# Optimization experiments

Measured on AMD Instinct MI355X. Metric: run time of the kernel, lower is better.

## Reference

```python
import jax, jax.numpy as jnp
import numpy as np

B, S, D = 2, 2048, 1024
H, DH = 16, 64  # num_head, head_dim; H*DH == D


def setup_inputs() -> dict:
    key = jax.random.key(0)
    ks = jax.random.split(key, 10)
    stdv = 1.0 / np.sqrt(D)
    def lin(k):
        kw, kb = jax.random.split(k)
        W = jax.random.uniform(kw, (D, D), jnp.float32, -stdv, stdv)
        b = jax.random.uniform(kb, (D,), jnp.float32, -stdv, stdv)
        return W, b
    Wq, bq = lin(ks[0]); Wk, bk = lin(ks[1]); Wv, bv = lin(ks[2]); Wo, bo = lin(ks[3])
    x = jax.random.normal(ks[4], (B, S, D), jnp.float32)
    # causal mask: True = attend
    mask = jnp.tril(jnp.ones((S, S), jnp.bool_))
    mask = jnp.broadcast_to(mask, (B, S, S))
    return {"x": x, "mask": mask, "Wq": Wq, "bq": bq, "Wk": Wk, "bk": bk,
            "Wv": Wv, "bv": bv, "Wo": Wo, "bo": bo}


def _split_head(t):
    # [B,S,D] -> [B*H, S, DH]
    return t.reshape(B, S, H, DH).transpose(0, 2, 1, 3).reshape(B * H, S, DH)


def _concat_head(t):
    # [B*H, S, DH] -> [B, S, D]
    return t.reshape(B, H, S, DH).transpose(0, 2, 1, 3).reshape(B, S, D)


def reference(x, mask, Wq, bq, Wk, bk, Wv, bv, Wo, bo):
    q = _split_head(x @ Wq.T + bq)
    k = _split_head(x @ Wk.T + bk)
    v = _split_head(x @ Wv.T + bv)
    scale = 1.0 / jnp.sqrt(jnp.float32(DH))
    # scores: [B, H, S, S], masked softmax (flash-attention math, unfused ref)
    scores = jnp.einsum('nqd,nkd->nqk', q, k).reshape(B, H, S, S) * scale
    scores = jnp.where(mask[:, None, :, :], scores, jnp.finfo(scores.dtype).min)
    attn = jax.nn.softmax(scores, axis=-1)
    out = jnp.einsum('bhqk,nkd->bhqd', attn, v.reshape(B, H, S, DH).reshape(B * H, S, DH)).reshape(B * H, S, DH) if False else jnp.einsum('nqk,nkd->nqd', attn.reshape(B * H, S, S), v)
    return _concat_head(out) @ Wo.T + bo
```

## Files before the change

### kernel.cpp

```cpp
#include <hip/hip_runtime.h>
#include <cstdint>

#define S_LEN  2048
#define NH     16
#define DHEAD  64
#define DMODEL 1024

typedef __bf16 bf16x8 __attribute__((ext_vector_type(8)));
typedef __bf16 bf16x2 __attribute__((ext_vector_type(2)));
typedef float  f32x4  __attribute__((ext_vector_type(4)));

__device__ __forceinline__ unsigned short f2bf(float x) {
  union { float f; unsigned int u; } c; c.f = x;
  unsigned int u = c.u;
  return (unsigned short)((u + 0x7fffu + ((u >> 16) & 1u)) >> 16);
}

__device__ __forceinline__ unsigned int pkbf(float a, float b) {
#if __has_builtin(__builtin_amdgcn_cvt_pk_bf16_f32)
  bf16x2 r = __builtin_amdgcn_cvt_pk_bf16_f32(a, b);
  return *(unsigned int*)&r;
#else
  return (unsigned int)f2bf(a) | ((unsigned int)f2bf(b) << 16);
#endif
}

__device__ __forceinline__ unsigned short f2bf1(float x) {
#if __has_builtin(__builtin_amdgcn_cvt_pk_bf16_f32)
  bf16x2 r = __builtin_amdgcn_cvt_pk_bf16_f32(x, x);
  union { bf16x2 v; unsigned int u; } c; c.v = r;
  return (unsigned short)(c.u & 0xffffu);
#else
  return f2bf(x);
#endif
}

__device__ __forceinline__ __bf16 us2bf(unsigned short u) {
  union { unsigned short u; __bf16 b; } c; c.u = u; return c.b;
}

__device__ __forceinline__ void glds16(const void* g, void* l) {
  __builtin_amdgcn_global_load_lds(
      (const __attribute__((address_space(1))) void*)g,
      (__attribute__((address_space(3))) void*)l, 16, 0, 0);
}

__device__ __forceinline__ f32x4 mfma16(bf16x8 a, bf16x8 b, f32x4 c) {
  return __builtin_amdgcn_mfma_f32_16x16x32_bf16(a, b, c, 0, 0, 0);
}

__global__ void cvt_all(const float* __restrict__ x,
                        const float* __restrict__ Wq,
                        const float* __restrict__ Wk,
                        const float* __restrict__ Wv,
                        const float* __restrict__ Wo,
                        unsigned short* __restrict__ xb,
                        unsigned short* __restrict__ wqkv,
                        unsigned short* __restrict__ wo) {
  const int b = blockIdx.x;
  const float* src;
  unsigned short* dst;
  int off;
  if (b < 4096)      { src = x;  dst = xb;                off = b; }
  else if (b < 5120) { src = Wq; dst = wqkv;              off = b - 4096; }
  else if (b < 6144) { src = Wk; dst = wqkv + (1 << 20);  off = b - 5120; }
  else if (b < 7168) { src = Wv; dst = wqkv + (2 << 20);  off = b - 6144; }
  else               { src = Wo; dst = wo;                off = b - 7168; }
  const int i = (off * 256 + threadIdx.x) * 4;
  float4 v = *(const float4*)&src[i];
  uint2 r;
  r.x = pkbf(v.x, v.y);
  r.y = pkbf(v.z, v.w);
  *(uint2*)&dst[i] = r;
}

template<int MODE, int BN>
__global__ __launch_bounds__(256)
void gemm_bt(const unsigned short* __restrict__ A,
             const unsigned short* __restrict__ W,
             const float* __restrict__ bias0,
             const float* __restrict__ bias1,
             const float* __restrict__ bias2,
             unsigned short* __restrict__ Qt,
             unsigned short* __restrict__ Kb,
             unsigned short* __restrict__ Vt,
             float* __restrict__ Out,
             int K) {
  constexpr int JN = BN / 32;
  __shared__ __align__(16) unsigned short As[2][128 * 32];
  __shared__ __align__(16) unsigned short Bs[2][BN * 32];
  const int t    = threadIdx.x;
  const int lane = t & 63;
  const int w    = t >> 6;
  const int lr   = lane & 15, lq = lane >> 4;
  const int wm   = (w >> 1) * 64, wn = (w & 1) * (BN / 2);
  const int m0   = blockIdx.y * 128, n0 = blockIdx.x * BN;
  const int ra   = t >> 2, ca = (t & 3) * 8;

  f32x4 acc[4][JN] = {};

  const int niter = K >> 6;
  for (int kk = 0; kk < niter; ++kk) {
    const int k0 = kk << 6;
#pragma unroll
    for (int kh = 0; kh < 2; ++kh) {
      const int kc = k0 + kh * 32;
      glds16(A + (m0 + ra) * K + kc + ca,      &As[kh][ra * 32 + ca]);
      glds16(A + (m0 + 64 + ra) * K + kc + ca, &As[kh][(64 + ra) * 32 + ca]);
      glds16(W + (n0 + ra) * K + kc + ca,      &Bs[kh][ra * 32 + ca]);
      if (BN == 128)
        glds16(W + (n0 + 64 + ra) * K + kc + ca, &Bs[kh][(64 + ra) * 32 + ca]);
    }
    __syncthreads();
#pragma unroll
    for (int kh = 0; kh < 2; ++kh) {
      bf16x8 af[4], bg[JN];
#pragma unroll
      for (int i = 0; i < 4; ++i)
        af[i] = *(const bf16x8*)&As[kh][(wm + i * 16 + lr) * 32 + lq * 8];
#pragma unroll
      for (int j = 0; j < JN; ++j)
        bg[j] = *(const bf16x8*)&Bs[kh][(wn + j * 16 + lr) * 32 + lq * 8];
#pragma unroll
      for (int i = 0; i < 4; ++i)
#pragma unroll
        for (int j = 0; j < JN; ++j)
          acc[i][j] = mfma16(af[i], bg[j], acc[i][j]);
    }
    __syncthreads();
  }

  if (MODE == 0) {
    const int tsel = n0 >> 10;
#pragma unroll
    for (int i = 0; i < 4; ++i) {
#pragma unroll
      for (int j = 0; j < JN; ++j) {
        const int mb = m0 + wm + i * 16 + lq * 4;
        const int n  = n0 + wn + j * 16 + lr;
        const int d  = n & 1023;
        const int bidx = mb >> 11, s = mb & (S_LEN - 1);
        const int h = d >> 6, dh = d & 63;
        const int bh = bidx * NH + h;
        const float bv0 = (tsel == 0) ? bias0[d] : ((tsel == 1) ? bias1[d] : bias2[d]);
        if (tsel == 0) {
          const float sc = 0.125f * 1.44269504088896f;
          uint2 pv;
          pv.x = pkbf((acc[i][j][0] + bv0) * sc, (acc[i][j][1] + bv0) * sc);
          pv.y = pkbf((acc[i][j][2] + bv0) * sc, (acc[i][j][3] + bv0) * sc);
          *(uint2*)&Qt[(bh * DHEAD + dh) * S_LEN + s] = pv;
        } else if (tsel == 2) {
          uint2 pv;
          pv.x = pkbf(acc[i][j][0] + bv0, acc[i][j][1] + bv0);
          pv.y = pkbf(acc[i][j][2] + bv0, acc[i][j][3] + bv0);
          *(uint2*)&Vt[(bh * DHEAD + dh) * S_LEN + s] = pv;
        } else {
#pragma unroll
          for (int r = 0; r < 4; ++r)
            Kb[(bh * S_LEN + s + r) * DHEAD + dh] = f2bf1(acc[i][j][r] + bv0);
        }
      }
    }
  } else {
#pragma unroll
    for (int i = 0; i < 4; ++i)
#pragma unroll
      for (int j = 0; j < JN; ++j)
#pragma unroll
        for (int r = 0; r < 4; ++r) {
          const int m = m0 + wm + i * 16 + lq * 4 + r;
          const int n = n0 + wn + j * 16 + lr;
          Out[m * DMODEL + n] = acc[i][j][r] + bias0[n];
        }
  }
}

__global__ __launch_bounds__(256, 2)
void flash_kernel(const unsigned short* __restrict__ Qt,
                  const unsigned short* __restrict__ Kb,
                  const unsigned short* __restrict__ Vt,
                  unsigned short* __restrict__ Ocat) {
  __shared__ __align__(16) unsigned short Ks[2][2][2][64 * 32];
  __shared__ __align__(16) unsigned short Vs[2][2][2][64 * 32];
  __shared__ __align__(16) unsigned short pls[4][1024];
  const int w = threadIdx.x >> 6, lane = threadIdx.x & 63;
  const int lr = lane & 15, lq = lane >> 4;
  const int bh = blockIdx.x;
  const int pp = blockIdx.y;
  const char* Kc = (const char*)(Kb + bh * (S_LEN * DHEAD));
  const char* Vc = (const char*)(Vt + bh * (DHEAD * S_LEN));
  const unsigned short* Qp = Qt + bh * (DHEAD * S_LEN);
  const int bb = bh >> 4, h = bh & 15;
  unsigned short* pw = &pls[w][0];
  const int swz = lr & 7;

  const int hh  = w & 1;
  const int rbb = (w >> 1) * 2;
  const int rlane = lane >> 2;
  const int slane = lane & 3;
  const int swslot = (slane ^ ((rlane >> 1) & 3)) * 16;
  const int rsw = (lq ^ ((lr >> 1) & 3)) * 8;

  bf16x8 ones;
#pragma unroll
  for (int j = 0; j < 8; ++j) ones[j] = (__bf16)1.0f;

  auto run_strip = [&](int sb) {
    const int nbt = (sb + 2) >> 1;
    const int q0 = sb * 64 + w * 16;
    bf16x8 qlo, qhi;
#pragma unroll
    for (int j = 0; j < 8; ++j) {
      qlo[j] = us2bf(Qp[(lq * 8 + j) * S_LEN + q0 + lr]);
      qhi[j] = us2bf(Qp[(32 + lq * 8 + j) * S_LEN + q0 + lr]);
    }
    f32x4 o[4] = {};
    f32x4 lacc = {};

    auto stage = [&](int buf, int bt) {
#pragma unroll
      for (int sub = 0; sub < 2; ++sub) {
        const int sk0 = bt * 128 + sub * 64;
#pragma unroll
        for (int j = 0; j < 2; ++j) {
          const int rb = rbb + j;
          glds16(Kc + (sk0 + rb * 16 + rlane) * 128 + hh * 64 + swslot,
                 &Ks[buf][sub][hh][rb * 16 * 32]);
          glds16(Vc + (rb * 16 + rlane) * 4096 + (sk0 + hh * 32) * 2 + swslot,
                 &Vs[buf][sub][hh][rb * 16 * 32]);
        }
      }
    };

    stage(0, 0);
    for (int bt = 0; bt < nbt; ++bt) {
      const int buf = bt & 1;
      __syncthreads();
      if (bt + 1 < nbt) stage(1 - buf, bt + 1);

#pragma unroll
      for (int sub = 0; sub < 2; ++sub) {
        f32x4 st[4] = {};
        const unsigned short* Kl = Ks[buf][sub][0];
        const unsigned short* Kh = Ks[buf][sub][1];
#pragma unroll
        for (int t = 0; t < 4; ++t) {
          st[t] = mfma16(*(const bf16x8*)&Kl[(t * 16 + lr) * 32 + rsw], qlo, st[t]);
          st[t] = mfma16(*(const bf16x8*)&Kh[(t * 16 + lr) * 32 + rsw], qhi, st[t]);
        }
        float p[4][4];
#pragma unroll
        for (int t = 0; t < 4; ++t)
#pragma unroll
          for (int r = 0; r < 4; ++r)
            p[t][r] = __builtin_amdgcn_exp2f(st[t][r]);
        if (bt == nbt - 1) {
          const int q = q0 + lr, sk0 = bt * 128 + sub * 64;
#pragma unroll
          for (int t = 0; t < 4; ++t)
#pragma unroll
            for (int r = 0; r < 4; ++r) {
              const int k = sk0 + t * 16 + lq * 4 + r;
              if (k > q) p[t][r] = 0.f;
            }
        }

#pragma unroll
        for (int t = 0; t < 4; ++t) {
          uint2 pk;
          pk.x = pkbf(p[t][0], p[t][1]);
          pk.y = pkbf(p[t][2], p[t][3]);
          const int g = t * 2 + (lq >> 1);
          *(uint2*)&pw[lr * 64 + ((g ^ swz) << 3) + ((lq & 1) << 2)] = pk;
        }
        const bf16x8 pf0 = *(const bf16x8*)&pw[lr * 64 + ((lq ^ swz) << 3)];
        const bf16x8 pf1 = *(const bf16x8*)&pw[lr * 64 + (((4 + lq) ^ swz) << 3)];
        const unsigned short* Vl = Vs[buf][sub][0];
        const unsigned short* Vh = Vs[buf][sub][1];
#pragma unroll
        for (int tt = 0; tt < 4; ++tt) {
          o[tt] = mfma16(*(const bf16x8*)&Vl[(tt * 16 + lr) * 32 + rsw], pf0, o[tt]);
          o[tt] = mfma16(*(const bf16x8*)&Vh[(tt * 16 + lr) * 32 + rsw], pf1, o[tt]);
        }
        lacc = mfma16(ones, pf0, lacc);
        lacc = mfma16(ones, pf1, lacc);
      }
    }

    const float inv = 1.f / lacc[0];
#pragma unroll
    for (int tt = 0; tt < 4; ++tt) {
      uint2 ov;
      ov.x = pkbf(o[tt][0] * inv, o[tt][1] * inv);
      ov.y = pkbf(o[tt][2] * inv, o[tt][3] * inv);
      *(uint2*)&Ocat[(bb * S_LEN + q0 + lr) * DMODEL + h * DHEAD + tt * 16 + lq * 4] = ov;
    }
    __syncthreads();
  };

  run_strip(31 - pp);
  run_strip(pp);
}

extern "C" void kernel_launch(void* const* d_in, const int* in_sizes, int n_in,
                              void* d_out, int out_size, void* d_ws, size_t ws_size,
                              hipStream_t stream) {
  const float* x  = (const float*)d_in[0];
  const float* Wq = (const float*)d_in[2];
  const float* bq = (const float*)d_in[3];
  const float* Wk = (const float*)d_in[4];
  const float* bk = (const float*)d_in[5];
  const float* Wv = (const float*)d_in[6];
  const float* bv = (const float*)d_in[7];
  const float* Wo = (const float*)d_in[8];
  const float* bo = (const float*)d_in[9];
  float* out = (float*)d_out;

  char* ws = (char*)d_ws;
  unsigned short* xb   = (unsigned short*)(ws);
  unsigned short* wqkv = (unsigned short*)(ws + (8ull  << 20));
  unsigned short* wo   = (unsigned short*)(ws + (14ull << 20));
  unsigned short* Qt   = (unsigned short*)(ws + (16ull << 20));
  unsigned short* Kb   = (unsigned short*)(ws + (24ull << 20));
  unsigned short* Vt   = (unsigned short*)(ws + (32ull << 20));
  unsigned short* Ocat = (unsigned short*)(ws + (40ull << 20));

  cvt_all<<<8192, 256, 0, stream>>>(x, Wq, Wk, Wv, Wo, xb, wqkv, wo);

  gemm_bt<0, 128><<<dim3(24, 32), 256, 0, stream>>>(xb, wqkv, bq, bk, bv,
                                                    Qt, Kb, Vt, nullptr, 1024);
  flash_kernel<<<dim3(32, 16), 256, 0, stream>>>(Qt, Kb, Vt, Ocat);
  gemm_bt<1, 64><<<dim3(16, 32), 256, 0, stream>>>(Ocat, wo, bo, nullptr, nullptr,
                                                   nullptr, nullptr, nullptr, out, 1024);
}
```

Before: 204.4 us.

## Split flash attention key tiles across warps and reduce partial outputs in LDS

```diff
diff --git a/kernel.cpp b/kernel.cpp
--- a/kernel.cpp
+++ b/kernel.cpp
@@ -180,9 +180,8 @@
                   const unsigned short* __restrict__ Kb,
                   const unsigned short* __restrict__ Vt,
                   unsigned short* __restrict__ Ocat) {
-  __shared__ __align__(16) unsigned short Ks[2][2][2][64 * 32];
-  __shared__ __align__(16) unsigned short Vs[2][2][2][64 * 32];
-  __shared__ __align__(16) unsigned short pls[4][1024];
+  __shared__ __align__(16) float Msh[4][64 * 64];
+  __shared__ float Ml[4][64];
   const int w = threadIdx.x >> 6, lane = threadIdx.x & 63;
   const int lr = lane & 15, lq = lane >> 4;
   const int bh = blockIdx.x;
@@ -191,62 +190,51 @@
   const char* Vc = (const char*)(Vt + bh * (DHEAD * S_LEN));
   const unsigned short* Qp = Qt + bh * (DHEAD * S_LEN);
   const int bb = bh >> 4, h = bh & 15;
-  unsigned short* pw = &pls[w][0];
+  unsigned short* pw = (unsigned short*)&Msh[w][0];
   const int swz = lr & 7;
 
-  const int hh  = w & 1;
-  const int rbb = (w >> 1) * 2;
-  const int rlane = lane >> 2;
-  const int slane = lane & 3;
-  const int swslot = (slane ^ ((rlane >> 1) & 3)) * 16;
-  const int rsw = (lq ^ ((lr >> 1) & 3)) * 8;
-
   bf16x8 ones;
 #pragma unroll
   for (int j = 0; j < 8; ++j) ones[j] = (__bf16)1.0f;
 
   auto run_strip = [&](int sb) {
-    const int nbt = (sb + 2) >> 1;
-    const int q0 = sb * 64 + w * 16;
-    bf16x8 qlo, qhi;
-#pragma unroll
-    for (int j = 0; j < 8; ++j) {
-      qlo[j] = us2bf(Qp[(lq * 8 + j) * S_LEN + q0 + lr]);
-      qhi[j] = us2bf(Qp[(32 + lq * 8 + j) * S_LEN + q0 + lr]);
-    }
-    f32x4 o[4] = {};
-    f32x4 lacc = {};
-
-    auto stage = [&](int buf, int bt) {
-#pragma unroll
-      for (int sub = 0; sub < 2; ++sub) {
-        const int sk0 = bt * 128 + sub * 64;
-#pragma unroll
-        for (int j = 0; j < 2; ++j) {
-          const int rb = rbb + j;
-          glds16(Kc + (sk0 + rb * 16 + rlane) * 128 + hh * 64 + swslot,
-                 &Ks[buf][sub][hh][rb * 16 * 32]);
-          glds16(Vc + (rb * 16 + rlane) * 4096 + (sk0 + hh * 32) * 2 + swslot,
-                 &Vs[buf][sub][hh][rb * 16 * 32]);
-        }
-      }
-    };
-
-    stage(0, 0);
-    for (int bt = 0; bt < nbt; ++bt) {
-      const int buf = bt & 1;
-      __syncthreads();
-      if (bt + 1 < nbt) stage(1 - buf, bt + 1);
-
-#pragma unroll
-      for (int sub = 0; sub < 2; ++sub) {
+    const int len = sb + 1;
+    const int q0 = sb * 64;
+    bf16x8 qlo[4], qhi[4];
+#pragma unroll
+    for (int qg = 0; qg < 4; ++qg)
+#pragma unroll
+      for (int j = 0; j < 8; ++j) {
+        qlo[qg][j] = us2bf(Qp[(lq * 8 + j) * S_LEN + q0 + qg * 16 + lr]);
+        qhi[qg][j] = us2bf(Qp[(32 + lq * 8 + j) * S_LEN + q0 + qg * 16 + lr]);
+      }
+    f32x4 o[4][4] = {};
+    f32x4 lacc[4] = {};
+
+    for (int kt = w; kt < len; kt += 4) {
+      const int sk0 = kt << 6;
+      bf16x8 kf0[4], kf1[4];
+#pragma unroll
+      for (int t = 0; t < 4; ++t) {
+        const char* kr = Kc + (sk0 + t * 16 + lr) * 128 + lq * 16;
+        kf0[t] = *(const bf16x8*)(kr);
+        kf1[t] = *(const bf16x8*)(kr + 64);
+      }
+      bf16x8 vf0[4], vf1[4];
+#pragma unroll
+      for (int tt = 0; tt < 4; ++tt) {
+        const char* vr = Vc + (tt * 16 + lr) * 4096 + sk0 * 2 + lq * 16;
+        vf0[tt] = *(const bf16x8*)(vr);
+        vf1[tt] = *(const bf16x8*)(vr + 64);
+      }
+      const bool diag = (kt == len - 1);
+#pragma unroll
+      for (int qg = 0; qg < 4; ++qg) {
         f32x4 st[4] = {};
-        const unsigned short* Kl = Ks[buf][sub][0];
-        const unsigned short* Kh = Ks[buf][sub][1];
 #pragma unroll
         for (int t = 0; t < 4; ++t) {
-          st[t] = mfma16(*(const bf16x8*)&Kl[(t * 16 + lr) * 32 + rsw], qlo, st[t]);
-          st[t] = mfma16(*(const bf16x8*)&Kh[(t * 16 + lr) * 32 + rsw], qhi, st[t]);
+          st[t] = mfma16(kf0[t], qlo[qg], st[t]);
+          st[t] = mfma16(kf1[t], qhi[qg], st[t]);
         }
         float p[4][4];
 #pragma unroll
@@ -254,8 +242,8 @@
 #pragma unroll
           for (int r = 0; r < 4; ++r)
             p[t][r] = __builtin_amdgcn_exp2f(st[t][r]);
-        if (bt == nbt - 1) {
-          const int q = q0 + lr, sk0 = bt * 128 + sub * 64;
+        if (diag) {
+          const int q = q0 + qg * 16 + lr;
 #pragma unroll
           for (int t = 0; t < 4; ++t)
 #pragma unroll
@@ -264,36 +252,53 @@
               if (k > q) p[t][r] = 0.f;
             }
         }
-
+        const int prow = (qg * 16 + lr) * 64;
 #pragma unroll
         for (int t = 0; t < 4; ++t) {
           uint2 pk;
           pk.x = pkbf(p[t][0], p[t][1]);
           pk.y = pkbf(p[t][2], p[t][3]);
           const int g = t * 2 + (lq >> 1);
-          *(uint2*)&pw[lr * 64 + ((g ^ swz) << 3) + ((lq & 1) << 2)] = pk;
-        }
-        const bf16x8 pf0 = *(const bf16x8*)&pw[lr * 64 + ((lq ^ swz) << 3)];
-        const bf16x8 pf1 = *(const bf16x8*)&pw[lr * 64 + (((4 + lq) ^ swz) << 3)];
-        const unsigned short* Vl = Vs[buf][sub][0];
-        const unsigned short* Vh = Vs[buf][sub][1];
+          *(uint2*)&pw[prow + ((g ^ swz) << 3) + ((lq & 1) << 2)] = pk;
+        }
+        const bf16x8 pf0 = *(const bf16x8*)&pw[prow + ((lq ^ swz) << 3)];
+        const bf16x8 pf1 = *(const bf16x8*)&pw[prow + (((4 + lq) ^ swz) << 3)];
 #pragma unroll
         for (int tt = 0; tt < 4; ++tt) {
-          o[tt] = mfma16(*(const bf16x8*)&Vl[(tt * 16 + lr) * 32 + rsw], pf0, o[tt]);
-          o[tt] = mfma16(*(const bf16x8*)&Vh[(tt * 16 + lr) * 32 + rsw], pf1, o[tt]);
-        }
-        lacc = mfma16(ones, pf0, lacc);
-        lacc = mfma16(ones, pf1, lacc);
-      }
-    }
-
-    const float inv = 1.f / lacc[0];
-#pragma unroll
-    for (int tt = 0; tt < 4; ++tt) {
+          o[qg][tt] = mfma16(vf0[tt], pf0, o[qg][tt]);
+          o[qg][tt] = mfma16(vf1[tt], pf1, o[qg][tt]);
+        }
+        lacc[qg] = mfma16(ones, pf0, lacc[qg]);
+        lacc[qg] = mfma16(ones, pf1, lacc[qg]);
+      }
+    }
+
+#pragma unroll
+    for (int qg = 0; qg < 4; ++qg) {
+#pragma unroll
+      for (int tt = 0; tt < 4; ++tt) {
+        const int slot = (tt * 4 + lq) ^ lr;
+        *(f32x4*)&Msh[w][(qg * 16 + lr) * 64 + slot * 4] = o[qg][tt];
+      }
+      if (lq == 0) Ml[w][qg * 16 + lr] = lacc[qg][0];
+    }
+    __syncthreads();
+    const int qrow = w * 16 + lr;
+    const float lt = Ml[0][qrow] + Ml[1][qrow] + Ml[2][qrow] + Ml[3][qrow];
+    const float inv = 1.f / lt;
+#pragma unroll
+    for (int m = 0; m < 4; ++m) {
+      const int slot = (m * 4 + lq) ^ lr;
+      f32x4 s = *(const f32x4*)&Msh[0][qrow * 64 + slot * 4];
+#pragma unroll
+      for (int v = 1; v < 4; ++v) {
+        f32x4 r = *(const f32x4*)&Msh[v][qrow * 64 + slot * 4];
+        s = s + r;
+      }
       uint2 ov;
-      ov.x = pkbf(o[tt][0] * inv, o[tt][1] * inv);
-      ov.y = pkbf(o[tt][2] * inv, o[tt][3] * inv);
-      *(uint2*)&Ocat[(bb * S_LEN + q0 + lr) * DMODEL + h * DHEAD + tt * 16 + lq * 4] = ov;
+      ov.x = pkbf(s[0] * inv, s[1] * inv);
+      ov.y = pkbf(s[2] * inv, s[3] * inv);
+      *(uint2*)&Ocat[(bb * S_LEN + q0 + qrow) * DMODEL + h * DHEAD + m * 16 + lq * 4] = ov;
     }
     __syncthreads();
   };
```

Result: no change. 208.0 us (+1.7%).
